# Optimization experiments

Hardware: AMD Instinct MI355X
Metric: run time of the kernel (lower is better)

The kernel has to match this reference:

```python
import jax, jax.numpy as jnp
import numpy as np

UNITS = 768
OUT_STEPS = 64
INPUT_DIM = 96


def setup_inputs() -> dict:
    key = jax.random.key(0)
    ks = jax.random.split(key, 7)
    B, T = 2048, 24
    s_ih = 1.0 / np.sqrt(UNITS)
    inputs = jax.random.normal(ks[0], (B, T, INPUT_DIM), dtype=jnp.float32)
    # PyTorch LSTMCell params: weight_ih [4U, I], weight_hh [4U, U], biases [4U]
    W_ih = jax.random.uniform(ks[1], (4 * UNITS, INPUT_DIM), minval=-s_ih, maxval=s_ih, dtype=jnp.float32)
    W_hh = jax.random.uniform(ks[2], (4 * UNITS, UNITS), minval=-s_ih, maxval=s_ih, dtype=jnp.float32)
    b_ih = jax.random.uniform(ks[3], (4 * UNITS,), minval=-s_ih, maxval=s_ih, dtype=jnp.float32)
    b_hh = jax.random.uniform(ks[4], (4 * UNITS,), minval=-s_ih, maxval=s_ih, dtype=jnp.float32)
    # Dense: Linear(units, input_dim)
    s_d = 1.0 / np.sqrt(UNITS)
    W_d = jax.random.uniform(ks[5], (INPUT_DIM, UNITS), minval=-s_d, maxval=s_d, dtype=jnp.float32)
    b_d = jax.random.uniform(ks[6], (INPUT_DIM,), minval=-s_d, maxval=s_d, dtype=jnp.float32)
    return {"inputs": inputs, "W_ih": W_ih, "W_hh": W_hh, "b_ih": b_ih, "b_hh": b_hh, "W_d": W_d, "b_d": b_d}


def _lstm_cell(x, h, c, W_ih, W_hh, b_ih, b_hh):
    # gates: [B, 4U], PyTorch gate order i, f, g, o
    gates = x @ W_ih.T + b_ih + h @ W_hh.T + b_hh
    i, f, g, o = jnp.split(gates, 4, axis=-1)
    i = jax.nn.sigmoid(i)
    f = jax.nn.sigmoid(f)
    g = jnp.tanh(g)
    o = jax.nn.sigmoid(o)
    c_new = f * c + i * g
    h_new = o * jnp.tanh(c_new)
    return h_new, c_new


def reference(inputs, W_ih, W_hh, b_ih, b_hh, W_d, b_d):
    B = inputs.shape[0]
    h0 = jnp.zeros((B, UNITS), dtype=inputs.dtype)
    c0 = jnp.zeros((B, UNITS), dtype=inputs.dtype)
    # warmup: feed last timestep
    x0 = inputs[:, -1, :]
    h, c = _lstm_cell(x0, h0, c0, W_ih, W_hh, b_ih, b_hh)
    pred0 = h @ W_d.T + b_d

    def step(carry, _):
        pred, h, c = carry
        h2, c2 = _lstm_cell(pred, h, c, W_ih, W_hh, b_ih, b_hh)
        pred2 = h2 @ W_d.T + b_d
        return (pred2, h2, c2), pred2

    _, preds_rest = jax.lax.scan(step, (pred0, h, c), None, length=OUT_STEPS - 1)
    # preds_rest: [out_steps-1, B, I] -> stack with pred0 along time axis 1
    preds = jnp.concatenate([pred0[None], preds_rest], axis=0)  # [out_steps, B, I]
    return jnp.transpose(preds, (1, 0, 2))  # [B, out_steps, I]
```

## Files before the change

### kernel.cpp

```cpp
#include <hip/hip_runtime.h>
#include <hip/hip_bf16.h>
#include <stdint.h>

typedef __hip_bfloat16 bf16_t;
typedef __attribute__((ext_vector_type(4))) float f32x4;
typedef __attribute__((ext_vector_type(8))) short s16x8;

#define UNITS 768
#define NCOLS 3072
#define NPRED 96
#define MROWS 2048

__device__ __forceinline__ float sigf(float x) {
    return __builtin_amdgcn_rcpf(1.f + __expf(-x));
}
__device__ __forceinline__ float tanh_fast(float x) {
    return 1.f - 2.f * __builtin_amdgcn_rcpf(1.f + __expf(2.f * x));
}


__global__ void prep_b0(const float* __restrict__ W_ih, bf16_t* __restrict__ B0T) {
    int idx = blockIdx.x * 256 + threadIdx.x;
    if (idx >= NCOLS * 96) return;
    int c = idx / 96, k = idx % 96;
    int u = ((c >> 6) << 4) + (c & 15);
    int g = (c >> 4) & 3;
    B0T[idx] = (bf16_t)W_ih[(g * UNITS + u) * 96 + k];
}

__global__ void prep_x0(const float* __restrict__ inputs, bf16_t* __restrict__ x0) {
    int idx = blockIdx.x * 256 + threadIdx.x;
    int j = idx & 7;
    int l = (idx >> 3) & 63;
    int fg = idx >> 9;
    int kf = fg % 3;
    int mf = fg / 3;
    int m = mf * 16 + (l & 15);
    int k = kf * 32 + (l >> 4) * 8 + j;
    x0[idx] = (bf16_t)inputs[(m * 24 + 23) * 96 + k];
}

__global__ void prep_bias(const float* __restrict__ b_ih, const float* __restrict__ b_hh,
                          const float* __restrict__ W_ih, const float* __restrict__ b_d,
                          float* __restrict__ b0_r, float* __restrict__ beff_r) {
    int c = blockIdx.x * 256 + threadIdx.x;
    if (c >= NCOLS) return;
    int u = ((c >> 6) << 4) + (c & 15);
    int g = (c >> 4) & 3;
    int r = g * UNITS + u;
    float v = b_ih[r] + b_hh[r];
    float acc = 0.f;
    for (int j = 0; j < 96; ++j) acc += W_ih[r * 96 + j] * b_d[j];
    b0_r[c] = v;
    beff_r[c] = v + acc;
}

__global__ void prep_beff2(const float* __restrict__ W_hh, const float* __restrict__ W_ih,
                           const float* __restrict__ W_d, bf16_t* __restrict__ BeffT) {
    __shared__ float sWih[64][96];
    __shared__ float sWd[96][64];
    const int c0 = blockIdx.x * 64, k0 = blockIdx.y * 64;
    const int tid = threadIdx.x;
    for (int i = tid; i < 64 * 96; i += 256) {
        int cc = i / 96, j = i % 96;
        int c = c0 + cc;
        int u = ((c >> 6) << 4) + (c & 15);
        int g = (c >> 4) & 3;
        sWih[cc][j] = W_ih[(g * UNITS + u) * 96 + j];
    }
    for (int i = tid; i < 96 * 64; i += 256) {
        int j = i / 64, kk = i % 64;
        sWd[j][kk] = W_d[j * UNITS + k0 + kk];
    }
    __syncthreads();
    const int kk = tid & 63;
    const int cc0 = (tid >> 6) * 16;
    for (int cc = cc0; cc < cc0 + 16; ++cc) {
        float acc = 0.f;
#pragma unroll 12
        for (int j = 0; j < 96; ++j) acc += sWih[cc][j] * sWd[j][kk];
        int c = c0 + cc;
        int u = ((c >> 6) << 4) + (c & 15);
        int g = (c >> 4) & 3;
        int r = g * UNITS + u;
        BeffT[(size_t)c * UNITS + k0 + kk] = (bf16_t)(W_hh[(size_t)r * UNITS + k0 + kk] + acc);
    }
}

__global__ void prep_wdt(const float* __restrict__ W_d, bf16_t* __restrict__ BeffT) {
    int idx = blockIdx.x * 256 + threadIdx.x;
    int c = idx / UNITS, k = idx % UNITS;
    float v = (c < NPRED) ? W_d[c * UNITS + k] : 0.f;
    BeffT[(size_t)(NCOLS + c) * UNITS + k] = (bf16_t)v;
}

__global__ void prep_swz(const bf16_t* __restrict__ src, bf16_t* __restrict__ dst,
                         int Knk, int K, int total) {
    int idx = blockIdx.x * 256 + threadIdx.x;
    if (idx >= total) return;
    int j = idx & 7;
    int l = (idx >> 3) & 63;
    int fg = idx >> 9;
    int f = fg & 3;
    int rest = fg >> 2;
    int kf = rest % Knk;
    int nw = rest / Knk;
    int c = (nw >> 1) * 128 + (nw & 1) * 64 + f * 16 + (l & 15);
    int k = kf * 32 + (l >> 4) * 8 + j;
    dst[idx] = src[(size_t)c * K + k];
}

__global__ void zero_ctr(int* __restrict__ c) {
    int i = blockIdx.x * 256 + threadIdx.x;
    if (i < 768) c[i] = 0;
}

__global__ __attribute__((amdgpu_flat_work_group_size(512, 512),
                          amdgpu_waves_per_eu(2, 2)))
void lstm_persist(const bf16_t* __restrict__ x0s,
                  const bf16_t* __restrict__ B0s,
                  const bf16_t* __restrict__ Bs,
                  const float* __restrict__ b0r,
                  const float* __restrict__ beffr,
                  const float* __restrict__ b_d,
                  bf16_t* __restrict__ h0,
                  bf16_t* __restrict__ h1,
                  float* __restrict__ out,
                  int* __restrict__ ctr)
{
    __shared__ __align__(16) bf16_t smem[24 * 6 * 512];
    __shared__ int sflag;

    const int tid = threadIdx.x;
    const int wv   = tid >> 6;
    const int lane = tid & 63;
    const int wr = wv >> 1, wc = wv & 1;
    const int l15 = lane & 15, l4 = lane >> 4;
    const int phB = (wv >> 2) & 1;

    const int bid  = blockIdx.x;
    const int grp  = bid & 7;
    const int tile = bid >> 3;
    const bool is_pred = (tile == 24);

    int xcc;
    asm volatile("s_getreg_b32 %0, hwreg(HW_REG_XCC_ID, 0, 4)" : "=s"(xcc));

    const bf16_t* Bg = Bs + (size_t)(2 * tile + wc) * 49152;

    {
        const f32x4* s0 = (const f32x4*)(Bs + (size_t)(2 * tile) * 49152);
        const f32x4* s1 = (const f32x4*)(Bs + (size_t)(2 * tile + 1) * 49152);
        f32x4* dst = (f32x4*)smem;
        for (int i = tid; i < 9216; i += 512) {
            int l  = i & 63;
            int ff = (i >> 6) % 6;
            int kf = i / 384;
            int f  = (ff >= 3) ? ff - 3 : ff;
            const f32x4* src = (ff >= 3) ? s1 : s0;
            dst[i] = src[(kf * 4 + f) * 64 + l];
        }
    }

    int* smask = ctr + 512;
    int* sctr  = ctr + 520;
    if (tid == 0) {
        __hip_atomic_fetch_or(smask + grp, 1 << (xcc & 15), __ATOMIC_RELAXED,
                              __HIP_MEMORY_SCOPE_AGENT);
        __hip_atomic_fetch_add(sctr + grp, 1, __ATOMIC_RELEASE,
                               __HIP_MEMORY_SCOPE_AGENT);
        int it = 0;
        while (__hip_atomic_load(sctr + grp, __ATOMIC_RELAXED,
                                 __HIP_MEMORY_SCOPE_AGENT) < 25) {
            __builtin_amdgcn_s_sleep(2);
            if (++it > (1 << 20)) break;
        }
        (void)__hip_atomic_load(sctr + grp, __ATOMIC_ACQUIRE,
                                __HIP_MEMORY_SCOPE_AGENT);
        int m = __hip_atomic_load(smask + grp, __ATOMIC_RELAXED,
                                  __HIP_MEMORY_SCOPE_AGENT);
        sflag = (__popc((unsigned)m) == 1) ? 1 : 0;
    }
    __syncthreads();
    const int fast = sflag;

    int aoffh[4], aoff0[4];
#pragma unroll
    for (int i = 0; i < 4; ++i) {
        int mf = grp * 16 + wr * 4 + i;
        aoffh[i] = (mf * 24) * 512 + lane * 8;
        aoff0[i] = (mf * 3) * 512 + lane * 8;
    }
    int boff0[4];
#pragma unroll
    for (int f = 0; f < 4; ++f)
        boff0[f] = (((2 * tile + wc) * 12 + f) * 64 + lane) * 8;

    const int ldsb = wc * 1536 + lane * 8;
    const int bgof = 1536 + lane * 8;

    float bi0[4], biS[4];
    if (!is_pred) {
#pragma unroll
        for (int f = 0; f < 4; ++f) {
            int idx = tile * 128 + wc * 64 + f * 16 + l15;
            bi0[f] = b0r[idx];
            biS[f] = beffr[idx];
        }
    } else {
#pragma unroll
        for (int f = 0; f < 4; ++f) {
            int j = wc * 64 + f * 16 + l15;
            biS[f] = (j < NPRED) ? b_d[j] : 0.f;
            bi0[f] = 0.f;
        }
    }

    const int kq = wc * 2 + (l15 >> 3);
    const int jj = l15 & 7;

    f32x4 creg[4];
#pragma unroll
    for (int i = 0; i < 4; ++i) creg[i] = f32x4{0.f, 0.f, 0.f, 0.f};

    int* cbase = ctr + grp * 64;

    f32x4 acc[4][4];

#define KM(T, OFF) ((((T) + (OFF)) < 24) ? ((T) + (OFF)) : ((T) + (OFF) - 24))

#define ZACC() do {                                                                  \
        _Pragma("unroll") for (int _i = 0; _i < 4; ++_i)                             \
        _Pragma("unroll") for (int _j = 0; _j < 4; ++_j)                             \
            acc[_i][_j] = f32x4{0.f, 0.f, 0.f, 0.f};                                 \
    } while (0)

#define LOADK_H(BUF, KT) do {                                                        \
        _Pragma("unroll")                                                            \
        for (int _i = 0; _i < 4; ++_i)                                               \
            afr[BUF][_i] = *(const s16x8*)(hA + aoffh[_i] + (size_t)(KT) * 512);     \
        _Pragma("unroll")                                                            \
        for (int _f = 0; _f < 3; ++_f)                                               \
            bfr[BUF][_f] = *(const s16x8*)(smem + ldsb + (KT) * 3072 + _f * 512);    \
        bfr[BUF][3] = *(const s16x8*)(Bg + bgof + (size_t)(KT) * 2048);              \
    } while (0)

#define LOADK_0(BUF, KT) do {                                                        \
        _Pragma("unroll")                                                            \
        for (int _i = 0; _i < 4; ++_i)                                               \
            afr[BUF][_i] = *(const s16x8*)(x0s + aoff0[_i] + (size_t)(KT) * 512);    \
        _Pragma("unroll")                                                            \
        for (int _f = 0; _f < 4; ++_f)                                               \
            bfr[BUF][_f] = *(const s16x8*)(B0s + boff0[_f] + (size_t)(KT) * 2048);   \
    } while (0)

#define MF(BUF) do {                                                                 \
        __builtin_amdgcn_s_setprio(1);                                               \
        _Pragma("unroll")                                                            \
        for (int _i = 0; _i < 4; ++_i)                                               \
            _Pragma("unroll")                                                        \
            for (int _j = 0; _j < 4; ++_j)                                           \
                acc[_i][_j] = __builtin_amdgcn_mfma_f32_16x16x32_bf16(               \
                    afr[BUF][_i], bfr[BUF][_j], acc[_i][_j], 0, 0, 0);               \
        __builtin_amdgcn_s_setprio(0);                                               \
    } while (0)

#define RUN4S(NK, LOADK, OFF) do {                                                   \
        s16x8 afr[4][4], bfr[4][4];                                                  \
        LOADK(0, KM(0, OFF));                                                        \
        if (1 < (NK)) LOADK(1, KM(1, OFF));                                          \
        if (2 < (NK)) LOADK(2, KM(2, OFF));                                          \
        _Pragma("unroll")                                                            \
        for (int _kt = 0; _kt < (NK); _kt += 4) {                                    \
            if (_kt + 3 < (NK)) LOADK(3, KM(_kt + 3, OFF));                          \
            MF(0);                                                                   \
            if (_kt + 4 < (NK)) LOADK(0, KM(_kt + 4, OFF));                          \
            if (_kt + 1 < (NK)) MF(1);                                               \
            if (_kt + 5 < (NK)) LOADK(1, KM(_kt + 5, OFF));                          \
            if (_kt + 2 < (NK)) MF(2);                                               \
            if (_kt + 6 < (NK)) LOADK(2, KM(_kt + 6, OFF));                          \
            if (_kt + 3 < (NK)) MF(3);                                               \
        }                                                                            \
    } while (0)

#define GATE_EPI(HW, BI) do {                                                        \
        _Pragma("unroll")                                                            \
        for (int _i = 0; _i < 4; ++_i) {                                             \
            const int _mf = grp * 16 + wr * 4 + _i;                                  \
            bf16_t* _hb = (HW) + (size_t)(_mf * 24 + tile) * 512;                    \
            _Pragma("unroll")                                                        \
            for (int _r = 0; _r < 4; ++_r) {                                         \
                float _gi = acc[_i][0][_r] + (BI)[0];                                \
                float _gf = acc[_i][1][_r] + (BI)[1];                                \
                float _gg = acc[_i][2][_r] + (BI)[2];                                \
                float _go = acc[_i][3][_r] + (BI)[3];                                \
                float _si = sigf(_gi);                                               \
                float _sf = sigf(_gf);                                               \
                float _tg = tanh_fast(_gg);                                          \
                float _so = sigf(_go);                                               \
                float _cn = _sf * creg[_i][_r] + _si * _tg;                          \
                creg[_i][_r] = _cn;                                                  \
                int _lp = (l4 * 4 + _r) | (kq << 4);                                 \
                _hb[_lp * 8 + jj] = (bf16_t)(_so * tanh_fast(_cn));                  \
            }                                                                        \
        }                                                                            \
    } while (0)

#define PRED_EPI(TCOL) do {                                                          \
        _Pragma("unroll")                                                            \
        for (int _f = 0; _f < 4; ++_f) {                                             \
            int _j = wc * 64 + _f * 16 + l15;                                        \
            if (_j < NPRED) {                                                        \
                _Pragma("unroll")                                                    \
                for (int _i = 0; _i < 4; ++_i)                                       \
                    _Pragma("unroll")                                                \
                    for (int _r = 0; _r < 4; ++_r) {                                 \
                        int _row = grp * 256 + wr * 64 + _i * 16 + l4 * 4 + _r;      \
                        out[((size_t)_row * 64 + (TCOL)) * NPRED + _j] =             \
                            acc[_i][_f][_r] + biS[_f];                               \
                    }                                                                \
            }                                                                        \
        }                                                                            \
    } while (0)

    auto barrier_step = [&](int s) {
        __syncthreads();
        if (fast) {
            if (tid == 0) {
                __hip_atomic_fetch_add(cbase + s, 1, __ATOMIC_RELAXED,
                                       __HIP_MEMORY_SCOPE_AGENT);
                int it = 0;
                while (__hip_atomic_load(cbase + s, __ATOMIC_RELAXED,
                                         __HIP_MEMORY_SCOPE_AGENT) < 25) {
                    __builtin_amdgcn_s_sleep(1);
                    if (++it > (1 << 20)) break;
                }
            }
            __syncthreads();
            asm volatile("buffer_inv" ::: "memory");
            asm volatile("s_waitcnt vmcnt(0)" ::: "memory");
        } else {
            if (tid == 0) {
                if (is_pred) {
                    __hip_atomic_fetch_add(cbase + s, 1, __ATOMIC_RELAXED,
                                           __HIP_MEMORY_SCOPE_AGENT);
                } else {
                    __hip_atomic_fetch_add(cbase + s, 1, __ATOMIC_RELEASE,
                                           __HIP_MEMORY_SCOPE_AGENT);
                }
                int it = 0;
                while (__hip_atomic_load(cbase + s, __ATOMIC_RELAXED,
                                         __HIP_MEMORY_SCOPE_AGENT) < 25) {
                    __builtin_amdgcn_s_sleep(4);
                    if (++it > (1 << 20)) break;
                }
                (void)__hip_atomic_load(cbase + s, __ATOMIC_ACQUIRE,
                                        __HIP_MEMORY_SCOPE_AGENT);
            }
            __syncthreads();
        }
    };

    if (!is_pred) {
        ZACC();
        RUN4S(3, LOADK_0, 0);
        GATE_EPI(h1, bi0);
    }
    barrier_step(0);

    for (int s = 1; s < 64; ++s) {
        const bf16_t* hA = (s & 1) ? h1 : h0;
        ZACC();
        if (phB) { RUN4S(24, LOADK_H, 12); }
        else     { RUN4S(24, LOADK_H, 0);  }
        if (!is_pred) {
            bf16_t* hW = ((s + 1) & 1) ? h1 : h0;
            GATE_EPI(hW, biS);
        } else {
            PRED_EPI(s - 1);
        }
        barrier_step(s);
    }

    if (is_pred) {
        const bf16_t* hA = h0;
        ZACC();
        if (phB) { RUN4S(24, LOADK_H, 12); }
        else     { RUN4S(24, LOADK_H, 0);  }
        PRED_EPI(63);
    }

#undef ZACC
#undef LOADK_H
#undef LOADK_0
#undef MF
#undef RUN4S
#undef KM
#undef GATE_EPI
#undef PRED_EPI
}

extern "C" void kernel_launch(void* const* d_in, const int* in_sizes, int n_in,
                              void* d_out, int out_size, void* d_ws, size_t ws_size,
                              hipStream_t stream)
{
    const float* inputs = (const float*)d_in[0];
    const float* W_ih   = (const float*)d_in[1];
    const float* W_hh   = (const float*)d_in[2];
    const float* b_ih   = (const float*)d_in[3];
    const float* b_hh   = (const float*)d_in[4];
    const float* W_d    = (const float*)d_in[5];
    const float* b_d    = (const float*)d_in[6];
    float* out = (float*)d_out;

    char* ws = (char*)d_ws;
    size_t off = 0;
    auto alloc = [&](size_t bytes) -> char* {
        char* p = ws + off;
        off = (off + bytes + 255) & ~(size_t)255;
        return p;
    };
    bf16_t* B0T   = (bf16_t*)alloc((size_t)NCOLS * 96 * 2);
    bf16_t* B0s   = (bf16_t*)alloc((size_t)NCOLS * 96 * 2);
    bf16_t* BeffT = (bf16_t*)alloc((size_t)3200 * UNITS * 2);
    bf16_t* Bs    = (bf16_t*)alloc((size_t)3200 * UNITS * 2);
    bf16_t* x0s   = (bf16_t*)alloc((size_t)MROWS * 96 * 2);
    bf16_t* h0    = (bf16_t*)alloc((size_t)MROWS * UNITS * 2);
    bf16_t* h1    = (bf16_t*)alloc((size_t)MROWS * UNITS * 2);
    float*  b0r   = (float*)alloc(NCOLS * 4);
    float*  beffr = (float*)alloc(NCOLS * 4);
    int*    ctr   = (int*)alloc(768 * 4);

    prep_b0   <<<(NCOLS * 96 + 255) / 256, 256, 0, stream>>>(W_ih, B0T);
    prep_swz  <<<(NCOLS * 96 + 255) / 256, 256, 0, stream>>>(B0T, B0s, 3, 96, NCOLS * 96);
    prep_x0   <<<(MROWS * 96) / 256, 256, 0, stream>>>(inputs, x0s);
    prep_bias <<<(NCOLS + 255) / 256, 256, 0, stream>>>(b_ih, b_hh, W_ih, b_d, b0r, beffr);
    prep_beff2<<<dim3(48, 12), 256, 0, stream>>>(W_hh, W_ih, W_d, BeffT);
    prep_wdt  <<<(128 * UNITS) / 256, 256, 0, stream>>>(W_d, BeffT);
    prep_swz  <<<(3200 * UNITS + 255) / 256, 256, 0, stream>>>(BeffT, Bs, 24, UNITS, 3200 * UNITS);
    zero_ctr  <<<3, 256, 0, stream>>>(ctr);

    lstm_persist<<<200, 512, 0, stream>>>(x0s, B0s, Bs, b0r, beffr, b_d,
                                          h0, h1, out, ctr);

    (void)ws_size; (void)in_sizes; (void)n_in; (void)out_size;
}
```

Before: 1.332 ms.

## Assign blocks to row groups by XCC so each group shares one die

Replaces the fixed blockIdx-based group/tile mapping with a dynamic claim scheme. Each block reads its XCC id and claims a tile within the group tied to that XCC, and overflow blocks fill the leftover slots. After a grid-wide barrier, a group is flagged fast only when all 25 of its blocks landed on one XCC. The aim is to keep per-group synchronisation and h-state exchange inside one XCC's L2 far more often than the old round-robin mapping allowed. The cost is an extra grid-wide startup barrier across all 200 blocks, which relies on every block being co-resident, and the claim counters must be zeroed before each launch.

```diff
diff --git a/kernel.cpp b/kernel.cpp
--- a/kernel.cpp
+++ b/kernel.cpp
@@ -129,7 +129,7 @@
                   int* __restrict__ ctr)
 {
     __shared__ __align__(16) bf16_t smem[24 * 6 * 512];
-    __shared__ int sflag;
+    __shared__ int sgrp, stile, sflag;
 
     const int tid = threadIdx.x;
     const int wv   = tid >> 6;
@@ -138,13 +138,54 @@
     const int l15 = lane & 15, l4 = lane >> 4;
     const int phB = (wv >> 2) & 1;
 
-    const int bid  = blockIdx.x;
-    const int grp  = bid & 7;
-    const int tile = bid >> 3;
-    const bool is_pred = (tile == 24);
-
     int xcc;
     asm volatile("s_getreg_b32 %0, hwreg(HW_REG_XCC_ID, 0, 4)" : "=s"(xcc));
+
+    int* claim  = ctr + 512;
+    int* gctr   = ctr + 524;
+    int* spillc = ctr + 525;
+
+    if (tid == 0) {
+        const int myx = xcc & 7;
+        int n = __hip_atomic_fetch_add(claim + myx, 1, __ATOMIC_RELAXED,
+                                       __HIP_MEMORY_SCOPE_AGENT);
+        __hip_atomic_fetch_add(gctr, 1, __ATOMIC_RELEASE,
+                               __HIP_MEMORY_SCOPE_AGENT);
+        int it = 0;
+        while (__hip_atomic_load(gctr, __ATOMIC_RELAXED,
+                                 __HIP_MEMORY_SCOPE_AGENT) < 200) {
+            __builtin_amdgcn_s_sleep(2);
+            if (++it > (1 << 20)) break;
+        }
+        (void)__hip_atomic_load(gctr, __ATOMIC_ACQUIRE,
+                                __HIP_MEMORY_SCOPE_AGENT);
+        int cl[8];
+        for (int g = 0; g < 8; ++g)
+            cl[g] = __hip_atomic_load(claim + g, __ATOMIC_RELAXED,
+                                      __HIP_MEMORY_SCOPE_AGENT);
+        int myg, myt;
+        if (n < 25) {
+            myg = myx; myt = n;
+        } else {
+            int k = __hip_atomic_fetch_add(spillc, 1, __ATOMIC_RELAXED,
+                                           __HIP_MEMORY_SCOPE_AGENT);
+            int idx = 0; myg = 0; myt = 24;
+            for (int g = 0; g < 8; ++g) {
+                int have = cl[g] < 25 ? cl[g] : 25;
+                for (int t = have; t < 25; ++t) {
+                    if (idx == k) { myg = g; myt = t; }
+                    ++idx;
+                }
+            }
+        }
+        sgrp = myg; stile = myt;
+        sflag = (cl[myg] >= 25) ? 1 : 0;
+    }
+    __syncthreads();
+    const int grp  = sgrp;
+    const int tile = stile;
+    const int fast = sflag;
+    const bool is_pred = (tile == 24);
 
     const bf16_t* Bg = Bs + (size_t)(2 * tile + wc) * 49152;
 
@@ -161,28 +202,6 @@
             dst[i] = src[(kf * 4 + f) * 64 + l];
         }
     }
-
-    int* smask = ctr + 512;
-    int* sctr  = ctr + 520;
-    if (tid == 0) {
-        __hip_atomic_fetch_or(smask + grp, 1 << (xcc & 15), __ATOMIC_RELAXED,
-                              __HIP_MEMORY_SCOPE_AGENT);
-        __hip_atomic_fetch_add(sctr + grp, 1, __ATOMIC_RELEASE,
-                               __HIP_MEMORY_SCOPE_AGENT);
-        int it = 0;
-        while (__hip_atomic_load(sctr + grp, __ATOMIC_RELAXED,
-                                 __HIP_MEMORY_SCOPE_AGENT) < 25) {
-            __builtin_amdgcn_s_sleep(2);
-            if (++it > (1 << 20)) break;
-        }
-        (void)__hip_atomic_load(sctr + grp, __ATOMIC_ACQUIRE,
-                                __HIP_MEMORY_SCOPE_AGENT);
-        int m = __hip_atomic_load(smask + grp, __ATOMIC_RELAXED,
-                                  __HIP_MEMORY_SCOPE_AGENT);
-        sflag = (__popc((unsigned)m) == 1) ? 1 : 0;
-    }
-    __syncthreads();
-    const int fast = sflag;
 
     int aoffh[4], aoff0[4];
 #pragma unroll
```

Measured after the change: 1.446 ms. +8.5%, slower.
